# Kernel tuning notes

Hardware: AMD Instinct MI355X
Metric: run time of the kernel (lower is better)

## Reference

```python
import jax, jax.numpy as jnp
import numpy as np

B, S, U, H = 4, 2048, 1024, 16
DH = U // H  # head dim = 64
EPS = 1e-8


def setup_inputs() -> dict:
    key = jax.random.key(0)
    ks = jax.random.split(key, 7)
    scale = 1.0 / np.sqrt(U)
    return {
        "queries": jax.random.normal(ks[0], (B, S, U), jnp.float32),
        "keys": jax.random.normal(ks[1], (B, S, U), jnp.float32),
        "values": jax.random.normal(ks[2], (B, S, U), jnp.float32),
        "Wq": jax.random.normal(ks[3], (U, U), jnp.float32) * scale,
        "bq": jnp.zeros((U,), jnp.float32),
        "Wk": jax.random.normal(ks[4], (U, U), jnp.float32) * scale,
        "bk": jnp.zeros((U,), jnp.float32),
        "Wv": jax.random.normal(ks[5], (U, U), jnp.float32) * scale,
        "bv": jnp.zeros((U,), jnp.float32),
        "Wr": jax.random.normal(ks[6], (U, U), jnp.float32) * scale,
        "br": jnp.zeros((U,), jnp.float32),
        "gamma": jnp.ones((U,), jnp.float32),
        "beta": jnp.zeros((U,), jnp.float32),
    }


def reference(queries, keys, values, Wq, bq, Wk, bk, Wv, bv, Wr, br, gamma, beta):
    relu = jax.nn.relu
    Q = relu(queries @ Wq + bq)           # [B,S,U]
    K = relu(keys @ Wk + bk)
    V = relu(values @ Wv + bv)
    V_res = relu(values @ Wr + br)        # residual branch

    # split heads: tf.split(axis=2) + concat(axis=0) == per-head attention
    Qh = Q.reshape(B, S, H, DH)
    Kh = K.reshape(B, S, H, DH)
    Vh = V.reshape(B, S, H, DH)

    scores = jnp.einsum("bshd,bthd->bhst", Qh, Kh) / jnp.sqrt(jnp.float32(DH))
    w = jax.nn.softmax(scores, axis=-1)   # dropout keep_prob=1 -> identity
    out = jnp.einsum("bhst,bthd->bshd", w, Vh).reshape(B, S, U)

    out = relu(out + V_res)

    # manual LayerNorm (eps inside sqrt)
    mean = jnp.mean(out, axis=-1, keepdims=True)
    var = jnp.mean(jnp.square(out - mean), axis=-1, keepdims=True)
    normalized = (out - mean) / jnp.sqrt(var + EPS)
    return gamma * normalized + beta
```

## Files before the change

kernel.cpp:

```cpp
#include <hip/hip_runtime.h>

constexpr int B = 4, S = 2048, U = 1024, H = 16, DH = 64;
constexpr int MTOT = B * S;
constexpr int NT = S / 64;

using bf16   = __bf16;
using f32x4  = __attribute__((ext_vector_type(4))) float;
using f32x16 = __attribute__((ext_vector_type(16))) float;
using bf16x8 = __attribute__((ext_vector_type(8))) bf16;
using bf16x4 = __attribute__((ext_vector_type(4))) bf16;
using u32x4  = __attribute__((ext_vector_type(4))) unsigned int;

__device__ __forceinline__ void gload16(const bf16* g, bf16* l) {
  __builtin_amdgcn_global_load_lds(
      (const __attribute__((address_space(1))) unsigned int*)g,
      (__attribute__((address_space(3))) unsigned int*)l, 16, 0, 0);
}

__device__ __forceinline__ float fexp2(float x) {
#if __has_builtin(__builtin_amdgcn_exp2f)
  return __builtin_amdgcn_exp2f(x);
#else
  return __expf(x * 0.6931471805599453f);
#endif
}

__device__ __forceinline__ f32x16 mfma32(bf16x8 a, bf16x8 b, f32x16 c) {
  return __builtin_amdgcn_mfma_f32_32x32x16_bf16(a, b, c, 0, 0, 0);
}

__device__ __forceinline__ unsigned packbf(float a, float b) {
  union { bf16 h; unsigned short s; } ua, ub;
  ua.h = (bf16)a; ub.h = (bf16)b;
  return ((unsigned)ub.s << 16) | (unsigned)ua.s;
}

__device__ __forceinline__ size_t kpack_off(int M_, int col) {
  const int b = M_ >> 11, s = M_ & 2047;
  const int h = col >> 6, d = col & 63;
  const int bh = b * 16 + h;
  const int t = s >> 6, r64 = s & 63;
  const int tt = r64 >> 5, l31 = r64 & 31;
  const int ks = d >> 4, hi = (d >> 3) & 1, j = d & 7;
  const int ln = l31 + (hi << 5);
  return ((size_t)(bh * 32 + t) << 12) + (tt << 11) + (ks << 9) + (ln << 3) + j;
}

__device__ __forceinline__ size_t vpack_off(int M_, int col) {
  const int b = M_ >> 11, s = M_ & 2047;
  const int h = col >> 6, d = col & 63;
  const int bh = b * 16 + h;
  const int j = s & 7, hi = (s >> 3) & 1, ks = (s >> 4) & 3, t = s >> 6;
  const int dt = d >> 5, l31 = d & 31;
  const int ln = l31 + (hi << 5);
  return ((size_t)(bh * 32 + t) << 12) + (dt << 11) + (ks << 9) + (ln << 3) + j;
}

__global__ __launch_bounds__(256) void prep_kernel(
    const float* __restrict__ xq, const float* __restrict__ xk, const float* __restrict__ xv,
    bf16* __restrict__ oq, bf16* __restrict__ ok, bf16* __restrict__ ov,
    const float* __restrict__ w0, const float* __restrict__ w1,
    const float* __restrict__ w2, const float* __restrict__ w3,
    bf16* __restrict__ t0, bf16* __restrict__ t1,
    bf16* __restrict__ t2, bf16* __restrict__ t3) {
  __shared__ float tile[32][33];
  const int bid = blockIdx.x;
  const int t = threadIdx.x;
  if (bid < 12288) {
    const int z = bid >> 12, idx = bid & 4095;
    const float* x = z == 0 ? xq : z == 1 ? xk : xv;
    bf16* o       = z == 0 ? oq : z == 1 ? ok : ov;
    const size_t i = ((size_t)idx * 256 + t) * 8;
    const float4 v0 = *reinterpret_cast<const float4*>(x + i);
    const float4 v1 = *reinterpret_cast<const float4*>(x + i + 4);
    bf16x8 r;
    r[0] = (bf16)v0.x; r[1] = (bf16)v0.y; r[2] = (bf16)v0.z; r[3] = (bf16)v0.w;
    r[4] = (bf16)v1.x; r[5] = (bf16)v1.y; r[6] = (bf16)v1.z; r[7] = (bf16)v1.w;
    *reinterpret_cast<bf16x8*>(o + i) = r;
  } else {
    const int wb = bid - 12288;
    const int z = wb >> 10, ti = wb & 1023;
    const float* W = z == 0 ? w0 : z == 1 ? w1 : z == 2 ? w2 : w3;
    bf16* Wt       = z == 0 ? t0 : z == 1 ? t1 : z == 2 ? t2 : t3;
    const int k0 = (ti & 31) * 32, n0 = (ti >> 5) * 32;
    const int tx = t & 31, ty = t >> 5;
    for (int i = ty; i < 32; i += 8) tile[i][tx] = W[(size_t)(k0 + i) * U + n0 + tx];
    __syncthreads();
    for (int i = ty; i < 32; i += 8) Wt[(size_t)(n0 + i) * U + k0 + tx] = (bf16)tile[tx][i];
  }
}

__global__ __launch_bounds__(256) void gemm4_kernel(
    const bf16* __restrict__ Qc, const bf16* __restrict__ Kc, const bf16* __restrict__ Vc,
    const bf16* __restrict__ wqt, const bf16* __restrict__ wkt,
    const bf16* __restrict__ wvt, const bf16* __restrict__ wrt,
    const float* __restrict__ bq, const float* __restrict__ bk,
    const float* __restrict__ bv, const float* __restrict__ br,
    bf16* __restrict__ oq, bf16* __restrict__ okp,
    bf16* __restrict__ ovp, bf16* __restrict__ orr) {
  const int bid = blockIdx.x;
  const int wg = (bid & 7) * 256 + (bid >> 3);
  const int z = wg >> 9, rem = wg & 511;
  const int bm = (rem >> 3) * 128, bn = (rem & 7) * 128;

  const bf16* A     = z == 0 ? Qc : z == 1 ? Kc : Vc;
  const bf16* Wt    = z == 0 ? wqt : z == 1 ? wkt : z == 2 ? wvt : wrt;
  const float* bias = z == 0 ? bq : z == 1 ? bk : z == 2 ? bv : br;

  const int t = threadIdx.x, lane = t & 63, wid = t >> 6;
  const int wr = wid >> 1, wc = wid & 1;
  const int lm = lane & 15, hi = lane >> 4;

  __shared__ __align__(16) bf16 As[128][64];
  __shared__ __align__(16) bf16 Bs[128][64];

  f32x4 acc[4][4];
#pragma unroll
  for (int i = 0; i < 4; ++i)
#pragma unroll
    for (int j = 0; j < 4; ++j) acc[i][j] = f32x4{0.f, 0.f, 0.f, 0.f};

  const int lr = lane >> 3;
  const int scol = ((lane & 7) ^ lr) * 8;
  const bf16* ga = A  + (size_t)(bm + wid * 32 + lr) * U + scol;
  const bf16* gb = Wt + (size_t)(bn + wid * 32 + lr) * U + scol;

  for (int k0 = 0; k0 < U; k0 += 64) {
    __syncthreads();
#pragma unroll
    for (int p = 0; p < 4; ++p) {
      gload16(ga + (size_t)(p * 8) * U + k0, &As[wid * 32 + p * 8][0]);
      gload16(gb + (size_t)(p * 8) * U + k0, &Bs[wid * 32 + p * 8][0]);
    }
    __syncthreads();

#pragma unroll
    for (int ksub = 0; ksub < 2; ++ksub) {
      const int so = (((ksub * 4 + hi) ^ (lm & 7)) * 16);
      bf16x8 a[4], bb[4];
#pragma unroll
      for (int mi = 0; mi < 4; ++mi)
        a[mi] = *reinterpret_cast<const bf16x8*>(
            reinterpret_cast<const char*>(&As[wr * 64 + mi * 16 + lm][0]) + so);
#pragma unroll
      for (int ni = 0; ni < 4; ++ni)
        bb[ni] = *reinterpret_cast<const bf16x8*>(
            reinterpret_cast<const char*>(&Bs[wc * 64 + ni * 16 + lm][0]) + so);
#pragma unroll
      for (int mi = 0; mi < 4; ++mi)
#pragma unroll
        for (int ni = 0; ni < 4; ++ni)
          acc[mi][ni] = __builtin_amdgcn_mfma_f32_16x16x32_bf16(a[mi], bb[ni], acc[mi][ni], 0, 0, 0);
    }
  }

  const int mb = bm + wr * 64 + hi * 4;
  const int nb = bn + wc * 64 + lm;
  if (z == 1) {
#pragma unroll
    for (int ni = 0; ni < 4; ++ni) {
      const float bv_ = bias[nb + ni * 16];
#pragma unroll
      for (int mi = 0; mi < 4; ++mi)
#pragma unroll
        for (int r = 0; r < 4; ++r) {
          const float vv = fmaxf(acc[mi][ni][r] + bv_, 0.f);
          okp[kpack_off(mb + mi * 16 + r, nb + ni * 16)] = (bf16)vv;
        }
    }
  } else if (z == 2) {
#pragma unroll
    for (int ni = 0; ni < 4; ++ni) {
      const float bv_ = bias[nb + ni * 16];
#pragma unroll
      for (int mi = 0; mi < 4; ++mi)
#pragma unroll
        for (int r = 0; r < 4; ++r) {
          const float vv = fmaxf(acc[mi][ni][r] + bv_, 0.f);
          ovp[vpack_off(mb + mi * 16 + r, nb + ni * 16)] = (bf16)vv;
        }
    }
  } else {
    bf16* out = z == 0 ? oq : orr;
#pragma unroll
    for (int ni = 0; ni < 4; ++ni) {
      const float bv_ = bias[nb + ni * 16];
#pragma unroll
      for (int mi = 0; mi < 4; ++mi)
#pragma unroll
        for (int r = 0; r < 4; ++r) {
          const float vv = fmaxf(acc[mi][ni][r] + bv_, 0.f);
          out[(size_t)(mb + mi * 16 + r) * U + nb + ni * 16] = (bf16)vv;
        }
    }
  }
}

__global__ __launch_bounds__(256, 2) void attn_kernel(
    const bf16* __restrict__ Q, const bf16* __restrict__ Kp,
    const bf16* __restrict__ Vp, bf16* __restrict__ att) {
  const int bid = blockIdx.x;
  const int swz = (bid & 7) * 128 + (bid >> 3);
  const int bh = swz >> 4, qx = swz & 15;
  const int b = bh >> 4, h = bh & 15;
  const int tid = threadIdx.x;
  const int w = tid >> 6, lane = tid & 63;
  const int l31 = lane & 31, hi8 = lane >> 5;
  const int q0 = qx * 128 + w * 32;

  __shared__ __align__(16) bf16 kv[2][8192];

  const float qscale = 0.18033688011111606f;

  const bf16* qbase = Q + ((size_t)b * S + q0 + l31) * U + h * DH + hi8 * 8;
  bf16x8 qf[4];
#pragma unroll
  for (int ks = 0; ks < 4; ++ks) {
    bf16x8 v = *reinterpret_cast<const bf16x8*>(qbase + ks * 16);
#pragma unroll
    for (int j = 0; j < 8; ++j) v[j] = (bf16)((float)v[j] * qscale);
    qf[ks] = v;
  }

  bf16x8 onesf;
#pragma unroll
  for (int j = 0; j < 8; ++j) onesf[j] = (bf16)1.f;

  f32x16 o0 = (f32x16)0.f, o1 = (f32x16)0.f, osum = (f32x16)0.f;

  const bf16* kpb = Kp + (size_t)bh * 32 * 4096;
  const bf16* vpb = Vp + (size_t)bh * 32 * 4096;

  auto stagekv = [&](int buf, int t) {
    const size_t toff = (size_t)t * 4096;
    gload16(kpb + toff + tid * 8,        &kv[buf][tid * 8]);
    gload16(kpb + toff + 2048 + tid * 8, &kv[buf][2048 + tid * 8]);
    gload16(vpb + toff + tid * 8,        &kv[buf][4096 + tid * 8]);
    gload16(vpb + toff + 2048 + tid * 8, &kv[buf][6144 + tid * 8]);
  };

  stagekv(0, 0);
  asm volatile("s_waitcnt vmcnt(0)" ::: "memory");
  __builtin_amdgcn_s_barrier();
  __builtin_amdgcn_sched_barrier(0);

  for (int t = 0; t < NT; ++t) {
    const int cur = t & 1;
    if (t + 1 < NT) stagekv(cur ^ 1, t + 1);

    bf16x8 kf[2][4];
#pragma unroll
    for (int tt = 0; tt < 2; ++tt)
#pragma unroll
      for (int ks = 0; ks < 4; ++ks)
        kf[tt][ks] = *reinterpret_cast<const bf16x8*>(&kv[cur][(tt * 4 + ks) * 512 + lane * 8]);

    f32x16 s0 = (f32x16)0.f, s1 = (f32x16)0.f;
    __builtin_amdgcn_s_setprio(1);
#pragma unroll
    for (int ks = 0; ks < 4; ++ks) {
      s0 = mfma32(kf[0][ks], qf[ks], s0);
      s1 = mfma32(kf[1][ks], qf[ks], s1);
    }
    __builtin_amdgcn_s_setprio(0);

    bf16x8 vf[2][4];
#pragma unroll
    for (int dt = 0; dt < 2; ++dt)
#pragma unroll
      for (int ks = 0; ks < 4; ++ks)
        vf[dt][ks] = *reinterpret_cast<const bf16x8*>(&kv[cur][4096 + (dt * 4 + ks) * 512 + lane * 8]);

    unsigned wpk[16];
#pragma unroll
    for (int i = 0; i < 8; ++i) {
      wpk[i]     = packbf(fexp2(s0[2 * i]), fexp2(s0[2 * i + 1]));
      wpk[8 + i] = packbf(fexp2(s1[2 * i]), fexp2(s1[2 * i + 1]));
    }

    u32x4 fw[4];
#pragma unroll
    for (int fi = 0; fi < 4; ++fi) {
      unsigned a0 = wpk[fi * 4 + 0], b0 = wpk[fi * 4 + 2];
      unsigned a1 = wpk[fi * 4 + 1], b1 = wpk[fi * 4 + 3];
      asm("v_permlane32_swap_b32 %0, %1" : "+v"(a0), "+v"(b0));
      asm("v_permlane32_swap_b32 %0, %1" : "+v"(a1), "+v"(b1));
      fw[fi] = u32x4{a0, a1, b0, b1};
    }

    __builtin_amdgcn_s_setprio(1);
#pragma unroll
    for (int ks = 0; ks < 4; ++ks) {
      const bf16x8 pf = __builtin_bit_cast(bf16x8, fw[ks]);
      o0   = mfma32(pf, vf[0][ks], o0);
      o1   = mfma32(pf, vf[1][ks], o1);
      osum = mfma32(pf, onesf, osum);
    }
    __builtin_amdgcn_s_setprio(0);

    if (t + 1 < NT) {
      asm volatile("s_waitcnt vmcnt(0)" ::: "memory");
      __builtin_amdgcn_s_barrier();
      __builtin_amdgcn_sched_barrier(0);
    }
  }

  bf16* obase = att + ((size_t)b * S + q0) * U + h * DH + l31;
#pragma unroll
  for (int r = 0; r < 16; ++r) {
    const int row = (r & 3) + 8 * (r >> 2) + 4 * hi8;
    const float lr = 1.f / osum[r];
    obase[(size_t)row * U]      = (bf16)(o0[r] * lr);
    obase[(size_t)row * U + 32] = (bf16)(o1[r] * lr);
  }
}

__global__ __launch_bounds__(256) void ln_kernel(
    const bf16* __restrict__ att, const bf16* __restrict__ vres,
    const float* __restrict__ gamma, const float* __restrict__ beta,
    float* __restrict__ out) {
  const int row = blockIdx.x;
  const int t = threadIdx.x;
  const bf16* ar = att + (size_t)row * U;
  const bf16* vr = vres + (size_t)row * U;
  const bf16x4 av = *reinterpret_cast<const bf16x4*>(ar + t * 4);
  const bf16x4 vv = *reinterpret_cast<const bf16x4*>(vr + t * 4);
  float x[4];
  float sum = 0.f, sq = 0.f;
#pragma unroll
  for (int i = 0; i < 4; ++i) {
    x[i] = fmaxf((float)av[i] + (float)vv[i], 0.f);
    sum += x[i];
    sq += x[i] * x[i];
  }
#pragma unroll
  for (int mm = 1; mm < 64; mm <<= 1) {
    sum += __shfl_xor(sum, mm);
    sq  += __shfl_xor(sq, mm);
  }
  __shared__ float s1[4], s2[4];
  if ((t & 63) == 0) { s1[t >> 6] = sum; s2[t >> 6] = sq; }
  __syncthreads();
  sum = s1[0] + s1[1] + s1[2] + s1[3];
  sq  = s2[0] + s2[1] + s2[2] + s2[3];
  const float mean = sum * (1.f / U);
  float var = sq * (1.f / U) - mean * mean;
  var = fmaxf(var, 0.f);
  const float inv = rsqrtf(var + 1e-8f);
#pragma unroll
  for (int i = 0; i < 4; ++i) {
    const int c = t * 4 + i;
    out[(size_t)row * U + c] = gamma[c] * ((x[i] - mean) * inv) + beta[c];
  }
}

extern "C" void kernel_launch(void* const* d_in, const int* in_sizes, int n_in,
                              void* d_out, int out_size, void* d_ws, size_t ws_size,
                              hipStream_t stream) {
  const float* queries = (const float*)d_in[0];
  const float* keys    = (const float*)d_in[1];
  const float* values  = (const float*)d_in[2];
  const float* Wq = (const float*)d_in[3];
  const float* bq = (const float*)d_in[4];
  const float* Wk = (const float*)d_in[5];
  const float* bk = (const float*)d_in[6];
  const float* Wv = (const float*)d_in[7];
  const float* bv = (const float*)d_in[8];
  const float* Wr = (const float*)d_in[9];
  const float* br = (const float*)d_in[10];
  const float* gamma = (const float*)d_in[11];
  const float* beta  = (const float*)d_in[12];
  float* out = (float*)d_out;

  char* ws = (char*)d_ws;
  const size_t MB = 1024 * 1024;
  bf16* wqt  = (bf16*)(ws + 0 * MB);
  bf16* wkt  = (bf16*)(ws + 2 * MB);
  bf16* wvt  = (bf16*)(ws + 4 * MB);
  bf16* wrt  = (bf16*)(ws + 6 * MB);
  bf16* Qcvt = (bf16*)(ws + 8 * MB);
  bf16* Kcvt = (bf16*)(ws + 24 * MB);
  bf16* Vcvt = (bf16*)(ws + 40 * MB);
  bf16* Qb   = (bf16*)(ws + 56 * MB);
  bf16* Kp   = (bf16*)(ws + 72 * MB);
  bf16* Vp   = (bf16*)(ws + 88 * MB);
  bf16* attb = Qcvt;
  bf16* Rb   = Kcvt;

  prep_kernel<<<dim3(16384), 256, 0, stream>>>(
      queries, keys, values, Qcvt, Kcvt, Vcvt,
      Wq, Wk, Wv, Wr, wqt, wkt, wvt, wrt);
  gemm4_kernel<<<dim3(2048), 256, 0, stream>>>(
      Qcvt, Kcvt, Vcvt, wqt, wkt, wvt, wrt, bq, bk, bv, br, Qb, Kp, Vp, Rb);
  attn_kernel<<<dim3(1024), 256, 0, stream>>>(Qb, Kp, Vp, attb);
  ln_kernel<<<dim3(MTOT), 256, 0, stream>>>(attb, Rb, gamma, beta, out);
}
```

Before: 206.4 us.

## Double-buffer projection GEMM LDS tiles with K=32 stages and manual waitcnt

Splits the projection GEMM's 64-wide K tile into two 32-wide LDS buffers and uses a ping-pong schedule. The global-to-LDS load for the next stage is issued while the current stage is computed, with explicit vmcnt/lgkmcnt waits and raw s_barrier calls in place of the two __syncthreads per iteration. The goal is to overlap global load latency with MFMA work. The cost is more barriers per K step and a new swizzle for the narrower rows, which could bring back LDS bank conflicts.

```diff
diff --git a/kernel.cpp b/kernel.cpp
--- a/kernel.cpp
+++ b/kernel.cpp
@@ -111,8 +111,8 @@
   const int wr = wid >> 1, wc = wid & 1;
   const int lm = lane & 15, hi = lane >> 4;
 
-  __shared__ __align__(16) bf16 As[128][64];
-  __shared__ __align__(16) bf16 Bs[128][64];
+  __shared__ __align__(16) bf16 As[2][128][32];
+  __shared__ __align__(16) bf16 Bs[2][128][32];
 
   f32x4 acc[4][4];
 #pragma unroll
@@ -120,38 +120,67 @@
 #pragma unroll
     for (int j = 0; j < 4; ++j) acc[i][j] = f32x4{0.f, 0.f, 0.f, 0.f};
 
-  const int lr = lane >> 3;
-  const int scol = ((lane & 7) ^ lr) * 8;
-  const bf16* ga = A  + (size_t)(bm + wid * 32 + lr) * U + scol;
-  const bf16* gb = Wt + (size_t)(bn + wid * 32 + lr) * U + scol;
+  const int srow = wid * 32 + (lane >> 2);
+  const int scol = ((lane & 3) ^ ((lane >> 3) & 3)) * 8;
+  const bf16* ga = A  + (size_t)(bm + srow) * U + scol;
+  const bf16* gb = Wt + (size_t)(bn + srow) * U + scol;
+
+  auto stage = [&](bf16 (*A_)[32], bf16 (*B_)[32], int k0) {
+    gload16(ga + k0,                  &A_[wid * 32][0]);
+    gload16(ga + (size_t)16 * U + k0, &A_[wid * 32 + 16][0]);
+    gload16(gb + k0,                  &B_[wid * 32][0]);
+    gload16(gb + (size_t)16 * U + k0, &B_[wid * 32 + 16][0]);
+  };
+
+  const int sw = (hi ^ ((lm >> 1) & 3)) * 8;
+
+  auto compute = [&](const bf16 (*A_)[32], const bf16 (*B_)[32]) {
+    bf16x8 a[4], bb[4];
+#pragma unroll
+    for (int mi = 0; mi < 4; ++mi)
+      a[mi] = *reinterpret_cast<const bf16x8*>(&A_[wr * 64 + mi * 16 + lm][sw]);
+#pragma unroll
+    for (int ni = 0; ni < 4; ++ni)
+      bb[ni] = *reinterpret_cast<const bf16x8*>(&B_[wc * 64 + ni * 16 + lm][sw]);
+#pragma unroll
+    for (int mi = 0; mi < 4; ++mi)
+#pragma unroll
+      for (int ni = 0; ni < 4; ++ni)
+        acc[mi][ni] = __builtin_amdgcn_mfma_f32_16x16x32_bf16(a[mi], bb[ni], acc[mi][ni], 0, 0, 0);
+  };
+
+  stage(As[0], Bs[0], 0);
+  asm volatile("s_waitcnt vmcnt(0)" ::: "memory");
+  __builtin_amdgcn_s_barrier();
+  __builtin_amdgcn_sched_barrier(0);
+  stage(As[1], Bs[1], 32);
 
   for (int k0 = 0; k0 < U; k0 += 64) {
-    __syncthreads();
-#pragma unroll
-    for (int p = 0; p < 4; ++p) {
-      gload16(ga + (size_t)(p * 8) * U + k0, &As[wid * 32 + p * 8][0]);
-      gload16(gb + (size_t)(p * 8) * U + k0, &Bs[wid * 32 + p * 8][0]);
-    }
-    __syncthreads();
-
-#pragma unroll
-    for (int ksub = 0; ksub < 2; ++ksub) {
-      const int so = (((ksub * 4 + hi) ^ (lm & 7)) * 16);
-      bf16x8 a[4], bb[4];
-#pragma unroll
-      for (int mi = 0; mi < 4; ++mi)
-        a[mi] = *reinterpret_cast<const bf16x8*>(
-            reinterpret_cast<const char*>(&As[wr * 64 + mi * 16 + lm][0]) + so);
-#pragma unroll
-      for (int ni = 0; ni < 4; ++ni)
-        bb[ni] = *reinterpret_cast<const bf16x8*>(
-            reinterpret_cast<const char*>(&Bs[wc * 64 + ni * 16 + lm][0]) + so);
-#pragma unroll
-      for (int mi = 0; mi < 4; ++mi)
-#pragma unroll
-        for (int ni = 0; ni < 4; ++ni)
-          acc[mi][ni] = __builtin_amdgcn_mfma_f32_16x16x32_bf16(a[mi], bb[ni], acc[mi][ni], 0, 0, 0);
-    }
+    compute(As[0], Bs[0]);
+    asm volatile("s_waitcnt lgkmcnt(0)" ::: "memory");
+    __builtin_amdgcn_s_barrier();
+    __builtin_amdgcn_sched_barrier(0);
+    if (k0 + 64 < U) {
+      stage(As[0], Bs[0], k0 + 64);
+      asm volatile("s_waitcnt vmcnt(4)" ::: "memory");
+    } else {
+      asm volatile("s_waitcnt vmcnt(0)" ::: "memory");
+    }
+    __builtin_amdgcn_s_barrier();
+    __builtin_amdgcn_sched_barrier(0);
+
+    compute(As[1], Bs[1]);
+    asm volatile("s_waitcnt lgkmcnt(0)" ::: "memory");
+    __builtin_amdgcn_s_barrier();
+    __builtin_amdgcn_sched_barrier(0);
+    if (k0 + 96 < U) {
+      stage(As[1], Bs[1], k0 + 96);
+      asm volatile("s_waitcnt vmcnt(4)" ::: "memory");
+    } else {
+      asm volatile("s_waitcnt vmcnt(0)" ::: "memory");
+    }
+    __builtin_amdgcn_s_barrier();
+    __builtin_amdgcn_sched_barrier(0);
   }
 
   const int mb = bm + wr * 64 + hi * 4;
```

New measurement: 232.6 us. +12.7%, slower.
